# Optimization experiments

Measured on AMD Instinct MI355X. Metric: run time of the kernel, lower is better.

## Reference

```python
import jax, jax.numpy as jnp
import numpy as np

EPS = 1e-5

def _conv(x, w, b):
    # NCHW x OIHW -> NCHW, stride 1, SAME padding (stencil center (1,1) of 3x3, or 1x1)
    y = jax.lax.conv_general_dilated(x, w, (1, 1), 'SAME',
                                     dimension_numbers=('NCHW', 'OIHW', 'NCHW'))
    return y + b[None, :, None, None]

def _bn(x, gamma, beta):
    # training-mode batchnorm: stats over (N, H, W) per channel
    mean = jnp.mean(x, axis=(0, 2, 3), keepdims=True)
    var = jnp.var(x, axis=(0, 2, 3), keepdims=True)
    xhat = (x - mean) * jax.lax.rsqrt(var + EPS)
    return xhat * gamma[None, :, None, None] + beta[None, :, None, None]

def setup_inputs() -> dict:
    key = jax.random.key(0)
    ks = jax.random.split(key, 12)
    B, Cin, Cout, H, W = 2, 64, 64, 512, 512
    s = 0.05
    return {
        'x':  jax.random.normal(ks[0], (B, Cin, H, W), jnp.float32),
        'w1': jax.random.normal(ks[1], (Cout, Cin, 3, 3), jnp.float32) * s,
        'b1': jnp.zeros((Cout,), jnp.float32),
        'g1': jnp.ones((Cout,), jnp.float32),
        'be1': jnp.zeros((Cout,), jnp.float32),
        'w2': jax.random.normal(ks[2], (Cout, Cout, 3, 3), jnp.float32) * s,
        'b2': jnp.zeros((Cout,), jnp.float32),
        'g2': jnp.ones((Cout,), jnp.float32),
        'be2': jnp.zeros((Cout,), jnp.float32),
        'wp': jax.random.normal(ks[3], (Cout, Cin, 1, 1), jnp.float32) * s,
        'bp': jnp.zeros((Cout,), jnp.float32),
        'gp': jnp.ones((Cout,), jnp.float32),
        'bep': jnp.zeros((Cout,), jnp.float32),
    }

def reference(x, w1, b1, g1, be1, w2, b2, g2, be2, wp, bp, gp, bep):
    # project branch: 1x1 conv ([(0,0)] stencil) + BN
    residual = _bn(_conv(x, wp, bp), gp, bep)
    # conv1: pad + 3x3 lattice conv (full cp stencil) + BN + Identity downsample + ReLU
    out = jax.nn.relu(_bn(_conv(x, w1, b1), g1, be1))
    # conv2: pad + 3x3 lattice conv + BN
    out = _bn(_conv(out, w2, b2), g2, be2)
    # residual add + output ReLU
    return jax.nn.relu(out + residual)
```

## Files before the change

### kernel.cpp

```cpp
#include <hip/hip_runtime.h>
#include <hip/hip_bf16.h>
#include <stdint.h>

typedef short short8 __attribute__((ext_vector_type(8)));
typedef float f32x4 __attribute__((ext_vector_type(4)));
typedef unsigned int u32;
typedef unsigned short u16;

#define HH 512
#define WW 512
#define CC 64
#define PLANE (HH*WW)
#define NSTATF 524288.0f

#define KTW 32
#define HSTR1 560
#define KBSTR1 1120
#define SLOTB1 4480
#define NSLOT 6
#define RING1 (NSLOT*SLOTB1)
#define BOUNCE1 16384
#define BOUNCE2 8192
#define NBC1 1024
#define K5S 132

__device__ __forceinline__ u16 f2bf(float f) {
  __hip_bfloat16 h = __float2bfloat16(f);
  return __builtin_bit_cast(u16, h);
}
__device__ __forceinline__ u32 pk2bf(float a, float b) {
  return (u32)f2bf(a) | ((u32)f2bf(b) << 16);
}
__device__ __forceinline__ float bf2f(u16 u) {
  u32 x = ((u32)u) << 16;
  return __builtin_bit_cast(float, x);
}
__device__ __forceinline__ int m6(int v) {
  v -= (v >= 6) ? 6 : 0;
  v -= (v >= 6) ? 6 : 0;
  return v;
}
__device__ __forceinline__ void lds_barrier() {
  asm volatile("s_waitcnt lgkmcnt(0)" ::: "memory");
  __builtin_amdgcn_s_barrier();
  __builtin_amdgcn_sched_barrier(0);
}

__global__ __launch_bounds__(512) void kprep(const float* __restrict__ w1,
    const float* __restrict__ w2, const float* __restrict__ wp,
    u16* __restrict__ wb1, u16* __restrict__ wb2, u16* __restrict__ wbp)
{
  const int id = blockIdx.x*512 + threadIdx.x;
  const int lane = id & 63;
  if (id < 9216) {
    const float* w = (id < 4608) ? w1 : w2;
    u16* o = (id < 4608) ? wb1 : wb2;
    const int fid = (id < 4608) ? (id >> 6) : ((id - 4608) >> 6);
    const int ct4 = fid / 18, rem = fid % 18;
    const int tap = rem >> 1, kb = rem & 1;
    const int cout = ct4*16 + (lane & 15);
    const int k0c = kb*32 + (lane >> 4)*8;
    u32 ow[4];
#pragma unroll
    for (int p = 0; p < 4; ++p) {
      ow[p] = pk2bf(w[(size_t)(cout*64 + k0c + p*2)*9 + tap],
                    w[(size_t)(cout*64 + k0c + p*2 + 1)*9 + tap]);
    }
    *(uint4*)(o + ((size_t)fid*64 + lane)*8) = make_uint4(ow[0],ow[1],ow[2],ow[3]);
  } else if (id < 9728) {
    const int fid = (id - 9216) >> 6;
    const int ct4 = fid >> 1, kb = fid & 1;
    const int cout = ct4*16 + (lane & 15);
    const int k0c = kb*32 + (lane >> 4)*8;
    u32 ow[4];
#pragma unroll
    for (int p = 0; p < 4; ++p)
      ow[p] = pk2bf(wp[cout*64 + k0c + p*2], wp[cout*64 + k0c + p*2 + 1]);
    *(uint4*)(wbp + ((size_t)fid*64 + lane)*8) = make_uint4(ow[0],ow[1],ow[2],ow[3]);
  }
}

__global__ __launch_bounds__(256) void k0(const float* __restrict__ x, u16* __restrict__ xh)
{
  __shared__ __align__(16) u32 Tp[32*260];
  const int tid = threadIdx.x;
  const int wt = blockIdx.x, h = blockIdx.y, n = blockIdx.z;
  const int w0 = wt*256;
  const float* xp = x + (size_t)n*CC*PLANE + (size_t)h*WW + w0;
#pragma unroll
  for (int it = 0; it < 8; ++it) {
    const int j = it*256 + tid;
    const int c2 = j >> 6, w4 = (j & 63) << 2;
    const f32x4 a = *(const f32x4*)(xp + (size_t)(c2*2    )*PLANE + w4);
    const f32x4 b = *(const f32x4*)(xp + (size_t)(c2*2 + 1)*PLANE + w4);
    uint4 o;
    o.x = pk2bf(a[0], b[0]);
    o.y = pk2bf(a[1], b[1]);
    o.z = pk2bf(a[2], b[2]);
    o.w = pk2bf(a[3], b[3]);
    *(uint4*)(Tp + (u32)c2*260 + (u32)(w4 ^ (4*(c2 >> 2)))) = o;
  }
  __syncthreads();
  u16* op = xh + ((size_t)(n*HH + h)*WW + w0)*CC;
#pragma unroll
  for (int it = 0; it < 8; ++it) {
    const int j = it*256 + tid;
    const int w = j >> 3, c8 = j & 7;
    const u32 wsw = (u32)(w ^ (4*c8));
    uint4 o;
    o.x = Tp[(u32)(c8*4 + 0)*260 + wsw];
    o.y = Tp[(u32)(c8*4 + 1)*260 + wsw];
    o.z = Tp[(u32)(c8*4 + 2)*260 + wsw];
    o.w = Tp[(u32)(c8*4 + 3)*260 + wsw];
    *(uint4*)(op + (size_t)w*CC + c8*8) = o;
  }
}

__global__ __launch_bounds__(256, 2) void kconv1(const u16* __restrict__ in,
    const u16* __restrict__ wb, const u16* __restrict__ wbp,
    u16* __restrict__ out, u16* __restrict__ yp,
    float* __restrict__ ps, float* __restrict__ pq,
    float* __restrict__ psp, float* __restrict__ pqp)
{
  __shared__ __align__(16) char LB[RING1 + BOUNCE1 + 512];
  const int tid = threadIdx.x;
  const int lane = tid & 63, wv = tid >> 6;
  const int l15 = lane & 15, lq = lane >> 4;
  const int wt = blockIdx.x, hs = blockIdx.y, n = blockIdx.z;
  const int w0 = wt*KTW, h0 = hs*16;
  const int bid = (n*32 + hs)*16 + wt;

  short8 wfr[18];
#pragma unroll
  for (int f = 0; f < 18; ++f)
    wfr[f] = *(const short8*)(wb + ((size_t)(wv*18 + f)*64 + lane)*8);
  short8 wpf[2];
#pragma unroll
  for (int kb = 0; kb < 2; ++kb)
    wpf[kb] = *(const short8*)(wbp + ((size_t)(wv*2 + kb)*64 + lane)*8);

  float s4[4] = {0,0,0,0}, q4[4] = {0,0,0,0};
  float sp4[4] = {0,0,0,0}, qp4[4] = {0,0,0,0};
  const u16* inb = in + (size_t)n*PLANE*CC;
  const u32 co0 = (u32)((lq >> 1)*KBSTR1 + (lq & 1)*HSTR1);
  const u32 co1 = co0 + 2*KBSTR1;

  auto ld_one = [&](int j, int cl, int c8) -> uint4 {
    const int gh = h0 - 1 + j, gw = w0 - 1 + cl;
    if (((u32)gh < (u32)HH) && ((u32)gw < (u32)WW))
      return *(const uint4*)(inb + ((size_t)gh*WW + gw)*CC + c8*8);
    return make_uint4(0u,0u,0u,0u);
  };
  auto st_one = [&](int slot, int cl, int c8, uint4 v) {
    *(uint4*)(LB + (size_t)slot*SLOTB1 + (c8>>1)*KBSTR1 + (c8&1)*HSTR1 + cl*16) = v;
  };

  for (int idx = tid; idx < 4*272; idx += 256) {
    const int jj = idx / 272, rem = idx - jj*272;
    st_one(jj, rem >> 3, rem & 7, ld_one(jj, rem >> 3, rem & 7));
  }
  __syncthreads();

  uint4 st0, st1, st2;
  auto issue2 = [&](int jb) {
    { const int idx = tid;       const int jj = idx/272, rem = idx - jj*272;
      st0 = ld_one(jb + jj, rem >> 3, rem & 7); }
    { const int idx = 256 + tid; const int jj = idx/272, rem = idx - jj*272;
      st1 = ld_one(jb + jj, rem >> 3, rem & 7); }
    if (tid < 32) { const int idx = 512 + tid; const int jj = idx/272, rem = idx - jj*272;
      st2 = ld_one(jb + jj, rem >> 3, rem & 7); }
  };
  auto write2 = [&](int jb) {
    { const int idx = tid;       const int jj = idx/272, rem = idx - jj*272;
      st_one(m6(jb + jj), rem >> 3, rem & 7, st0); }
    { const int idx = 256 + tid; const int jj = idx/272, rem = idx - jj*272;
      st_one(m6(jb + jj), rem >> 3, rem & 7, st1); }
    if (tid < 32) { const int idx = 512 + tid; const int jj = idx/272, rem = idx - jj*272;
      st_one(m6(jb + jj), rem >> 3, rem & 7, st2); }
  };

  issue2(4);

  for (int g = 0; g < 8; ++g) {
    if (g > 0) write2(2*g + 2);
    lds_barrier();
    if (g < 7) issue2(2*g + 4);

    const char* sb[4];
#pragma unroll
    for (int mi = 0; mi < 4; ++mi)
      sb[mi] = LB + (size_t)m6(2*g + mi)*SLOTB1 + l15*16;
    f32x4 a0t0, a0t1, a1t0, a1t1;
    f32x4 p0t0, p0t1, p1t0, p1t1;
#pragma unroll
    for (int r = 0; r < 4; ++r) {
      a0t0[r]=0.f; a0t1[r]=0.f; a1t0[r]=0.f; a1t1[r]=0.f;
      p0t0[r]=0.f; p0t1[r]=0.f; p1t0[r]=0.f; p1t1[r]=0.f;
    }
#pragma unroll
    for (int t = 0; t < 2; ++t) {
      const int pb = t*16;
#pragma unroll
      for (int kb = 0; kb < 2; ++kb) {
        const u32 ck = kb ? co1 : co0;
#pragma unroll
        for (int mi = 0; mi < 4; ++mi) {
#pragma unroll
          for (int kw = 0; kw < 3; ++kw) {
            const short8 X = *(const short8*)(sb[mi] + ck + (u32)((pb + kw)*16));
            if (mi <= 2) {
              const short8 Wf = wfr[(mi*3 + kw)*2 + kb];
              if (t == 0) a0t0 = __builtin_amdgcn_mfma_f32_16x16x32_bf16(Wf, X, a0t0, 0,0,0);
              else        a0t1 = __builtin_amdgcn_mfma_f32_16x16x32_bf16(Wf, X, a0t1, 0,0,0);
            }
            if (mi >= 1) {
              const short8 Wf = wfr[((mi-1)*3 + kw)*2 + kb];
              if (t == 0) a1t0 = __builtin_amdgcn_mfma_f32_16x16x32_bf16(Wf, X, a1t0, 0,0,0);
              else        a1t1 = __builtin_amdgcn_mfma_f32_16x16x32_bf16(Wf, X, a1t1, 0,0,0);
            }
            if (kw == 1 && mi == 1) {
              if (t == 0) p0t0 = __builtin_amdgcn_mfma_f32_16x16x32_bf16(wpf[kb], X, p0t0, 0,0,0);
              else        p0t1 = __builtin_amdgcn_mfma_f32_16x16x32_bf16(wpf[kb], X, p0t1, 0,0,0);
            }
            if (kw == 1 && mi == 2) {
              if (t == 0) p1t0 = __builtin_amdgcn_mfma_f32_16x16x32_bf16(wpf[kb], X, p1t0, 0,0,0);
              else        p1t1 = __builtin_amdgcn_mfma_f32_16x16x32_bf16(wpf[kb], X, p1t1, 0,0,0);
            }
          }
        }
      }
    }
    {
      const int co = wv*16 + lq*4;
#pragma unroll
      for (int r = 0; r < 4; ++r) {
        s4[r] += a0t0[r] + a0t1[r] + a1t0[r] + a1t1[r];
        q4[r] = fmaf(a0t0[r], a0t0[r], q4[r]);
        q4[r] = fmaf(a0t1[r], a0t1[r], q4[r]);
        q4[r] = fmaf(a1t0[r], a1t0[r], q4[r]);
        q4[r] = fmaf(a1t1[r], a1t1[r], q4[r]);
        sp4[r] += p0t0[r] + p0t1[r] + p1t0[r] + p1t1[r];
        qp4[r] = fmaf(p0t0[r], p0t0[r], qp4[r]);
        qp4[r] = fmaf(p0t1[r], p0t1[r], qp4[r]);
        qp4[r] = fmaf(p1t0[r], p1t0[r], qp4[r]);
        qp4[r] = fmaf(p1t1[r], p1t1[r], qp4[r]);
      }
#pragma unroll
      for (int t = 0; t < 2; ++t) {
        const int pos = t*16 + l15;
        const u32 addr = ((u32)(pos*128 + co*2)) ^ (((u32)(pos & 7)) << 4);
        uint2 c0, c1, d0, d1;
        if (t == 0) {
          c0.x = pk2bf(a0t0[0], a0t0[1]); c0.y = pk2bf(a0t0[2], a0t0[3]);
          c1.x = pk2bf(a1t0[0], a1t0[1]); c1.y = pk2bf(a1t0[2], a1t0[3]);
          d0.x = pk2bf(p0t0[0], p0t0[1]); d0.y = pk2bf(p0t0[2], p0t0[3]);
          d1.x = pk2bf(p1t0[0], p1t0[1]); d1.y = pk2bf(p1t0[2], p1t0[3]);
        } else {
          c0.x = pk2bf(a0t1[0], a0t1[1]); c0.y = pk2bf(a0t1[2], a0t1[3]);
          c1.x = pk2bf(a1t1[0], a1t1[1]); c1.y = pk2bf(a1t1[2], a1t1[3]);
          d0.x = pk2bf(p0t1[0], p0t1[1]); d0.y = pk2bf(p0t1[2], p0t1[3]);
          d1.x = pk2bf(p1t1[0], p1t1[1]); d1.y = pk2bf(p1t1[2], p1t1[3]);
        }
        *(uint2*)(LB + RING1 + 0*4096 + addr) = c0;
        *(uint2*)(LB + RING1 + 1*4096 + addr) = c1;
        *(uint2*)(LB + RING1 + 2*4096 + addr) = d0;
        *(uint2*)(LB + RING1 + 3*4096 + addr) = d1;
      }
    }
    lds_barrier();
    {
      const int rowi = tid >> 6, tt = tid & 63;
      const int pos = tt >> 1, half = (tt & 1)*64;
      const char* bb = LB + RING1 + rowi*4096;
      u16* base = (rowi < 2) ? out : yp;
      const int orow = h0 + 2*g + (rowi & 1);
      char* dst = (char*)base + ((size_t)((n*HH + orow)*WW + w0 + pos))*128 + half;
      const u32 sw = ((u32)(pos & 7)) << 4;
#pragma unroll
      for (int k2 = 0; k2 < 4; ++k2) {
        const uint4 v = *(const uint4*)(bb + (((u32)(pos*128 + half + k2*16)) ^ sw));
        *(uint4*)(dst + k2*16) = v;
      }
    }
  }

#pragma unroll
  for (int d = 1; d <= 8; d <<= 1) {
#pragma unroll
    for (int r = 0; r < 4; ++r) {
      s4[r] += __shfl_xor(s4[r], d, 64);
      q4[r] += __shfl_xor(q4[r], d, 64);
      sp4[r] += __shfl_xor(sp4[r], d, 64);
      qp4[r] += __shfl_xor(qp4[r], d, 64);
    }
  }
  if (l15 == 0) {
#pragma unroll
    for (int r = 0; r < 4; ++r) {
      const int co = wv*16 + lq*4 + r;
      ps[(size_t)co*NBC1 + bid] = s4[r];
      pq[(size_t)co*NBC1 + bid] = q4[r];
      psp[(size_t)co*NBC1 + bid] = sp4[r];
      pqp[(size_t)co*NBC1 + bid] = qp4[r];
    }
  }
}

__global__ __launch_bounds__(256, 2) void kconv2(const u16* __restrict__ in,
    const u16* __restrict__ wb,
    const float* __restrict__ As, const float* __restrict__ Bs,
    u16* __restrict__ out, float* __restrict__ ps, float* __restrict__ pq)
{
  __shared__ __align__(16) char LB[RING1 + BOUNCE2 + 512];
  float* sA = (float*)(LB + RING1 + BOUNCE2);
  float* sB = sA + 64;
  const int tid = threadIdx.x;
  const int lane = tid & 63, wv = tid >> 6;
  const int l15 = lane & 15, lq = lane >> 4;
  const int wt = blockIdx.x, hs = blockIdx.y, n = blockIdx.z;
  const int w0 = wt*KTW, h0 = hs*16;
  const int bid = (n*32 + hs)*16 + wt;

  if (tid < 64) { sA[tid] = As[tid]; sB[tid] = Bs[tid]; }
  __syncthreads();

  short8 wfr[18];
#pragma unroll
  for (int f = 0; f < 18; ++f)
    wfr[f] = *(const short8*)(wb + ((size_t)(wv*18 + f)*64 + lane)*8);

  float s4[4] = {0,0,0,0}, q4[4] = {0,0,0,0};
  const u16* inb = in + (size_t)n*PLANE*CC;
  const u32 co0 = (u32)((lq >> 1)*KBSTR1 + (lq & 1)*HSTR1);
  const u32 co1 = co0 + 2*KBSTR1;

  auto ld_one = [&](int j, int cl, int c8) -> uint4 {
    const int gh = h0 - 1 + j, gw = w0 - 1 + cl;
    if (((u32)gh < (u32)HH) && ((u32)gw < (u32)WW))
      return *(const uint4*)(inb + ((size_t)gh*WW + gw)*CC + c8*8);
    return make_uint4(0u,0u,0u,0u);
  };
  auto st_one = [&](int slot, int cl, int c8, uint4 v) {
    const u32* uw = (const u32*)&v;
    u32 ow[4];
    const int cb = c8*8;
#pragma unroll
    for (int h2 = 0; h2 < 4; ++h2) {
      float f0 = fmaxf(bf2f((u16)(uw[h2] & 0xFFFFu)) * sA[cb+h2*2]   + sB[cb+h2*2],   0.f);
      float f1 = fmaxf(bf2f((u16)(uw[h2] >> 16))     * sA[cb+h2*2+1] + sB[cb+h2*2+1], 0.f);
      ow[h2] = pk2bf(f0, f1);
    }
    *(uint4*)(LB + (size_t)slot*SLOTB1 + (c8>>1)*KBSTR1 + (c8&1)*HSTR1 + cl*16) =
        make_uint4(ow[0],ow[1],ow[2],ow[3]);
  };

  for (int idx = tid; idx < 4*272; idx += 256) {
    const int jj = idx / 272, rem = idx - jj*272;
    st_one(jj, rem >> 3, rem & 7, ld_one(jj, rem >> 3, rem & 7));
  }
  __syncthreads();

  uint4 st0, st1, st2;
  auto issue2 = [&](int jb) {
    { const int idx = tid;       const int jj = idx/272, rem = idx - jj*272;
      st0 = ld_one(jb + jj, rem >> 3, rem & 7); }
    { const int idx = 256 + tid; const int jj = idx/272, rem = idx - jj*272;
      st1 = ld_one(jb + jj, rem >> 3, rem & 7); }
    if (tid < 32) { const int idx = 512 + tid; const int jj = idx/272, rem = idx - jj*272;
      st2 = ld_one(jb + jj, rem >> 3, rem & 7); }
  };
  auto write2 = [&](int jb) {
    { const int idx = tid;       const int jj = idx/272, rem = idx - jj*272;
      st_one(m6(jb + jj), rem >> 3, rem & 7, st0); }
    { const int idx = 256 + tid; const int jj = idx/272, rem = idx - jj*272;
      st_one(m6(jb + jj), rem >> 3, rem & 7, st1); }
    if (tid < 32) { const int idx = 512 + tid; const int jj = idx/272, rem = idx - jj*272;
      st_one(m6(jb + jj), rem >> 3, rem & 7, st2); }
  };

  issue2(4);

  for (int g = 0; g < 8; ++g) {
    if (g > 0) write2(2*g + 2);
    lds_barrier();
    if (g < 7) issue2(2*g + 4);

    const char* sb[4];
#pragma unroll
    for (int mi = 0; mi < 4; ++mi)
      sb[mi] = LB + (size_t)m6(2*g + mi)*SLOTB1 + l15*16;
    f32x4 a0t0, a0t1, a1t0, a1t1;
#pragma unroll
    for (int r = 0; r < 4; ++r) { a0t0[r]=0.f; a0t1[r]=0.f; a1t0[r]=0.f; a1t1[r]=0.f; }
#pragma unroll
    for (int t = 0; t < 2; ++t) {
      const int pb = t*16;
#pragma unroll
      for (int kb = 0; kb < 2; ++kb) {
        const u32 ck = kb ? co1 : co0;
#pragma unroll
        for (int mi = 0; mi < 4; ++mi) {
#pragma unroll
          for (int kw = 0; kw < 3; ++kw) {
            const short8 X = *(const short8*)(sb[mi] + ck + (u32)((pb + kw)*16));
            if (mi <= 2) {
              const short8 Wf = wfr[(mi*3 + kw)*2 + kb];
              if (t == 0) a0t0 = __builtin_amdgcn_mfma_f32_16x16x32_bf16(Wf, X, a0t0, 0,0,0);
              else        a0t1 = __builtin_amdgcn_mfma_f32_16x16x32_bf16(Wf, X, a0t1, 0,0,0);
            }
            if (mi >= 1) {
              const short8 Wf = wfr[((mi-1)*3 + kw)*2 + kb];
              if (t == 0) a1t0 = __builtin_amdgcn_mfma_f32_16x16x32_bf16(Wf, X, a1t0, 0,0,0);
              else        a1t1 = __builtin_amdgcn_mfma_f32_16x16x32_bf16(Wf, X, a1t1, 0,0,0);
            }
          }
        }
      }
    }
    {
      const int co = wv*16 + lq*4;
#pragma unroll
      for (int r = 0; r < 4; ++r) {
        s4[r] += a0t0[r] + a0t1[r] + a1t0[r] + a1t1[r];
        q4[r] = fmaf(a0t0[r], a0t0[r], q4[r]);
        q4[r] = fmaf(a0t1[r], a0t1[r], q4[r]);
        q4[r] = fmaf(a1t0[r], a1t0[r], q4[r]);
        q4[r] = fmaf(a1t1[r], a1t1[r], q4[r]);
      }
#pragma unroll
      for (int t = 0; t < 2; ++t) {
        const int pos = t*16 + l15;
        const u32 addr = ((u32)(pos*128 + co*2)) ^ (((u32)(pos & 7)) << 4);
        uint2 c0, c1;
        if (t == 0) {
          c0.x = pk2bf(a0t0[0], a0t0[1]); c0.y = pk2bf(a0t0[2], a0t0[3]);
          c1.x = pk2bf(a1t0[0], a1t0[1]); c1.y = pk2bf(a1t0[2], a1t0[3]);
        } else {
          c0.x = pk2bf(a0t1[0], a0t1[1]); c0.y = pk2bf(a0t1[2], a0t1[3]);
          c1.x = pk2bf(a1t1[0], a1t1[1]); c1.y = pk2bf(a1t1[2], a1t1[3]);
        }
        *(uint2*)(LB + RING1 + 0*4096 + addr) = c0;
        *(uint2*)(LB + RING1 + 1*4096 + addr) = c1;
      }
    }
    lds_barrier();
    {
      const int rowi = tid >> 7, tt = tid & 127;
      const int pos = tt >> 2, qb = (tt & 3)*32;
      const char* bb = LB + RING1 + rowi*4096;
      const u32 a0 = ((u32)(pos*128 + qb)) ^ (((u32)(pos & 7)) << 4);
      const uint4 v0 = *(const uint4*)(bb + a0);
      const uint4 v1 = *(const uint4*)(bb + (a0 ^ 16u));
      char* dst = (char*)out + ((size_t)((n*HH + h0 + 2*g + rowi)*WW + w0 + pos))*128 + qb;
      *(uint4*)dst = v0;
      *(uint4*)(dst + 16) = v1;
    }
  }

#pragma unroll
  for (int d = 1; d <= 8; d <<= 1) {
#pragma unroll
    for (int r = 0; r < 4; ++r) {
      s4[r] += __shfl_xor(s4[r], d, 64);
      q4[r] += __shfl_xor(q4[r], d, 64);
    }
  }
  if (l15 == 0) {
#pragma unroll
    for (int r = 0; r < 4; ++r) {
      const int co = wv*16 + lq*4 + r;
      ps[(size_t)co*NBC1 + bid] = s4[r];
      pq[(size_t)co*NBC1 + bid] = q4[r];
    }
  }
}

__global__ __launch_bounds__(256) void kfin2(
    const float* __restrict__ psA, const float* __restrict__ pqA,
    const float* __restrict__ gA, const float* __restrict__ beA,
    float* __restrict__ AA, float* __restrict__ BA, int cntA,
    const float* __restrict__ psB, const float* __restrict__ pqB,
    const float* __restrict__ gB, const float* __restrict__ beB,
    float* __restrict__ AB, float* __restrict__ BB, int cntB)
{
  const int blk = blockIdx.x;
  const bool second = blk >= 64;
  const int c = blk & 63;
  const float* psx = second ? psB : psA;
  const float* pqx = second ? pqB : pqA;
  const float* g  = second ? gB  : gA;
  const float* be = second ? beB : beA;
  float* A  = second ? AB : AA;
  float* Bc = second ? BB : BA;
  const int cnt = second ? cntB : cntA;

  const int t = threadIdx.x;
  float sv = 0.f, s2 = 0.f;
  const float* pr = psx + (size_t)c*cnt;
  const float* qr = pqx + (size_t)c*cnt;
  for (int k = t; k < cnt; k += 256) { sv += pr[k]; s2 += qr[k]; }
#pragma unroll
  for (int d = 1; d < 64; d <<= 1) { sv += __shfl_xor(sv, d, 64); s2 += __shfl_xor(s2, d, 64); }
  __shared__ float as_[4], aq_[4];
  if ((t & 63) == 0) { as_[t >> 6] = sv; aq_[t >> 6] = s2; }
  __syncthreads();
  if (t == 0) {
    sv = as_[0] + as_[1] + as_[2] + as_[3];
    s2 = aq_[0] + aq_[1] + aq_[2] + aq_[3];
    const float mean = sv / NSTATF;
    const float var = s2 / NSTATF - mean*mean;
    const float istd = rsqrtf(var + 1e-5f);
    const float a = g[c] * istd;
    A[c] = a;
    Bc[c] = be[c] - mean * a;
  }
}

__global__ __launch_bounds__(256) void k5(const u16* __restrict__ y2, const u16* __restrict__ yp,
    const float* __restrict__ A2, const float* __restrict__ B2c,
    const float* __restrict__ Ap, const float* __restrict__ Bp,
    float* __restrict__ outp)
{
  __shared__ float T[CC*K5S];
  __shared__ float cA2[64], cB2[64], cAp[64], cBp[64];
  const int tid = threadIdx.x;
  const int lane = tid & 63, wv = tid >> 6;
  const int wt = blockIdx.x, h = blockIdx.y, n = blockIdx.z;
  const int w0 = wt*128;
  if (tid < 64) { cA2[tid] = A2[tid]; cB2[tid] = B2c[tid]; cAp[tid] = Ap[tid]; cBp[tid] = Bp[tid]; }
  __syncthreads();
  const u16* p2 = y2 + ((size_t)(n*HH + h)*WW + w0)*CC;
  const u16* pp = yp + ((size_t)(n*HH + h)*WW + w0)*CC;
#pragma unroll
  for (int it = 0; it < 4; ++it) {
    const int j = it*256 + tid;
    const int w = j >> 3, c8 = j & 7;
    const uint4 u2 = *(const uint4*)(p2 + (size_t)w*CC + c8*8);
    const uint4 up = *(const uint4*)(pp + (size_t)w*CC + c8*8);
    const u32* m2 = (const u32*)&u2;
    const u32* mp = (const u32*)&up;
    const u32 sw = ((u32)(c8 & 3)) << 3;
#pragma unroll
    for (int h2 = 0; h2 < 4; ++h2) {
      const int c = c8*8 + h2*2;
      const float a = bf2f((u16)(m2[h2] & 0xFFFFu)), b = bf2f((u16)(m2[h2] >> 16));
      const float ra = bf2f((u16)(mp[h2] & 0xFFFFu)), rb = bf2f((u16)(mp[h2] >> 16));
      const u32 wsw = (u32)w ^ sw;
      T[(u32)(c    )*K5S + wsw] = fmaxf(a*cA2[c]   + cB2[c]   + ra*cAp[c]   + cBp[c],   0.f);
      T[(u32)(c + 1)*K5S + wsw] = fmaxf(b*cA2[c+1] + cB2[c+1] + rb*cAp[c+1] + cBp[c+1], 0.f);
    }
  }
  __syncthreads();
#pragma unroll
  for (int cc = 0; cc < 16; ++cc) {
    const int c = cc*4 + wv;
    const u32 sw = ((u32)((c >> 3) & 3)) << 3;
    const u32 idx = (u32)c*K5S + (((u32)(lane*2)) ^ sw);
    float2 v;
    v.x = T[idx];
    v.y = T[idx + 1];
    *(float2*)(outp + ((size_t)((n*CC + c)*HH + h))*WW + w0 + lane*2) = v;
  }
}

extern "C" void kernel_launch(void* const* d_in, const int* in_sizes, int n_in,
                              void* d_out, int out_size, void* d_ws, size_t ws_size,
                              hipStream_t stream)
{
  (void)in_sizes; (void)n_in; (void)out_size;
  const float* x   = (const float*)d_in[0];
  const float* w1  = (const float*)d_in[1];
  const float* g1  = (const float*)d_in[3];
  const float* be1 = (const float*)d_in[4];
  const float* w2  = (const float*)d_in[5];
  const float* g2  = (const float*)d_in[7];
  const float* be2 = (const float*)d_in[8];
  const float* wp  = (const float*)d_in[9];
  const float* gp  = (const float*)d_in[11];
  const float* bep = (const float*)d_in[12];

  const size_t TENB = (size_t)2*CC*PLANE*2;
  char* ws = (char*)d_ws;
  u16* bufA = (u16*)ws;
  u16* bufB = (u16*)(ws + TENB);
  u16* bufC = (u16*)(ws + TENB*2);
  char* aux = ws + TENB*3;
  u16* wb1 = (u16*)aux;
  u16* wb2 = (u16*)(aux + 73728);
  u16* wbp = (u16*)(aux + 147456);
  float* ps1 = (float*)(aux + 155648);
  float* pq1 = ps1 + 64*NBC1;
  float* psp = pq1 + 64*NBC1;
  float* pqp = psp + 64*NBC1;
  float* ps2 = pqp + 64*NBC1;
  float* pq2 = ps2 + 64*NBC1;
  float* A1  = pq2 + 64*NBC1;
  float* B1  = A1 + 64;
  float* A2  = B1 + 64;
  float* B2c = A2 + 64;
  float* Ap  = B2c + 64;
  float* Bp  = Ap + 64;
  const size_t need = (size_t)(Bp + 64 - (float*)ws) * 4;
  if (ws_size < need) return;

  kprep<<<19, 512, 0, stream>>>(w1, w2, wp, wb1, wb2, wbp);
  k0<<<dim3(2, HH, 2), 256, 0, stream>>>(x, bufA);
  kconv1<<<dim3(16, 32, 2), 256, 0, stream>>>(bufA, wb1, wbp,
                                              bufB, bufC, ps1, pq1, psp, pqp);
  kfin2<<<128, 256, 0, stream>>>(ps1, pq1, g1, be1, A1, B1, NBC1,
                                 psp, pqp, gp, bep, Ap, Bp, NBC1);
  kconv2<<<dim3(16, 32, 2), 256, 0, stream>>>(bufB, wb2, A1, B1,
                                              bufA, ps2, pq2);
  kfin2<<<64, 256, 0, stream>>>(ps2, pq2, g2, be2, A2, B2c, NBC1,
                                ps2, pq2, g2, be2, A2, B2c, NBC1);
  k5<<<dim3(4, HH, 2), 256, 0, stream>>>(bufA, bufC, A2, B2c, Ap, Bp, (float*)d_out);
}
```

Measured before the change: 216.3 us.

## Recompute 1x1 projection in final kernel instead of storing it

The projection conv output is no longer written to a global buffer in kconv1. Instead, k5 reloads the bf16 NHWC input and recomputes the 1x1 conv with MFMA before the fused BN/residual/ReLU epilogue. kconv2 now writes to bufC so bufA (the transposed input) stays live. This trades a full-size bf16 write and read of the projection tensor for a re-read of the input plus a small amount of extra matrix work and more LDS use in k5.

```diff
diff --git a/kernel.cpp b/kernel.cpp
--- a/kernel.cpp
+++ b/kernel.cpp
@@ -19,8 +19,7 @@
 #define SLOTB1 4480
 #define NSLOT 6
 #define RING1 (NSLOT*SLOTB1)
-#define BOUNCE1 16384
-#define BOUNCE2 8192
+#define BOUNCE 8192
 #define NBC1 1024
 #define K5S 132
 
@@ -118,11 +117,11 @@
 
 __global__ __launch_bounds__(256, 2) void kconv1(const u16* __restrict__ in,
     const u16* __restrict__ wb, const u16* __restrict__ wbp,
-    u16* __restrict__ out, u16* __restrict__ yp,
+    u16* __restrict__ out,
     float* __restrict__ ps, float* __restrict__ pq,
     float* __restrict__ psp, float* __restrict__ pqp)
 {
-  __shared__ __align__(16) char LB[RING1 + BOUNCE1 + 512];
+  __shared__ __align__(16) char LB[RING1 + BOUNCE + 512];
   const int tid = threadIdx.x;
   const int lane = tid & 63, wv = tid >> 6;
   const int l15 = lane & 15, lq = lane >> 4;
@@ -249,38 +248,29 @@
       for (int t = 0; t < 2; ++t) {
         const int pos = t*16 + l15;
         const u32 addr = ((u32)(pos*128 + co*2)) ^ (((u32)(pos & 7)) << 4);
-        uint2 c0, c1, d0, d1;
+        uint2 c0, c1;
         if (t == 0) {
           c0.x = pk2bf(a0t0[0], a0t0[1]); c0.y = pk2bf(a0t0[2], a0t0[3]);
           c1.x = pk2bf(a1t0[0], a1t0[1]); c1.y = pk2bf(a1t0[2], a1t0[3]);
-          d0.x = pk2bf(p0t0[0], p0t0[1]); d0.y = pk2bf(p0t0[2], p0t0[3]);
-          d1.x = pk2bf(p1t0[0], p1t0[1]); d1.y = pk2bf(p1t0[2], p1t0[3]);
         } else {
           c0.x = pk2bf(a0t1[0], a0t1[1]); c0.y = pk2bf(a0t1[2], a0t1[3]);
           c1.x = pk2bf(a1t1[0], a1t1[1]); c1.y = pk2bf(a1t1[2], a1t1[3]);
-          d0.x = pk2bf(p0t1[0], p0t1[1]); d0.y = pk2bf(p0t1[2], p0t1[3]);
-          d1.x = pk2bf(p1t1[0], p1t1[1]); d1.y = pk2bf(p1t1[2], p1t1[3]);
         }
         *(uint2*)(LB + RING1 + 0*4096 + addr) = c0;
         *(uint2*)(LB + RING1 + 1*4096 + addr) = c1;
-        *(uint2*)(LB + RING1 + 2*4096 + addr) = d0;
-        *(uint2*)(LB + RING1 + 3*4096 + addr) = d1;
       }
     }
     lds_barrier();
     {
-      const int rowi = tid >> 6, tt = tid & 63;
-      const int pos = tt >> 1, half = (tt & 1)*64;
+      const int rowi = tid >> 7, tt = tid & 127;
+      const int pos = tt >> 2, qb = (tt & 3)*32;
       const char* bb = LB + RING1 + rowi*4096;
-      u16* base = (rowi < 2) ? out : yp;
-      const int orow = h0 + 2*g + (rowi & 1);
-      char* dst = (char*)base + ((size_t)((n*HH + orow)*WW + w0 + pos))*128 + half;
-      const u32 sw = ((u32)(pos & 7)) << 4;
-#pragma unroll
-      for (int k2 = 0; k2 < 4; ++k2) {
-        const uint4 v = *(const uint4*)(bb + (((u32)(pos*128 + half + k2*16)) ^ sw));
-        *(uint4*)(dst + k2*16) = v;
-      }
+      const u32 a0 = ((u32)(pos*128 + qb)) ^ (((u32)(pos & 7)) << 4);
+      const uint4 v0 = *(const uint4*)(bb + a0);
+      const uint4 v1 = *(const uint4*)(bb + (a0 ^ 16u));
+      char* dst = (char*)out + ((size_t)((n*HH + h0 + 2*g + rowi)*WW + w0 + pos))*128 + qb;
+      *(uint4*)dst = v0;
+      *(uint4*)(dst + 16) = v1;
     }
   }
 
@@ -311,8 +301,8 @@
     const float* __restrict__ As, const float* __restrict__ Bs,
     u16* __restrict__ out, float* __restrict__ ps, float* __restrict__ pq)
 {
-  __shared__ __align__(16) char LB[RING1 + BOUNCE2 + 512];
-  float* sA = (float*)(LB + RING1 + BOUNCE2);
+  __shared__ __align__(16) char LB[RING1 + BOUNCE + 512];
+  float* sA = (float*)(LB + RING1 + BOUNCE);
   float* sB = sA + 64;
   const int tid = threadIdx.x;
   const int lane = tid & 63, wv = tid >> 6;
@@ -516,27 +506,67 @@
   }
 }
 
-__global__ __launch_bounds__(256) void k5(const u16* __restrict__ y2, const u16* __restrict__ yp,
+__global__ __launch_bounds__(256) void k5(const u16* __restrict__ y2, const u16* __restrict__ xh,
+    const u16* __restrict__ wbp,
     const float* __restrict__ A2, const float* __restrict__ B2c,
     const float* __restrict__ Ap, const float* __restrict__ Bp,
     float* __restrict__ outp)
 {
-  __shared__ float T[CC*K5S];
-  __shared__ float cA2[64], cB2[64], cAp[64], cBp[64];
+  __shared__ __align__(16) char L5[50176 + 1024];
+  float* T = (float*)L5;
+  char* SG = L5;
+  char* BN = L5 + 33792;
+  float* cA2 = (float*)(L5 + 50176);
+  float* cB2 = cA2 + 64;
+  float* cAp = cB2 + 64;
+  float* cBp = cAp + 64;
   const int tid = threadIdx.x;
   const int lane = tid & 63, wv = tid >> 6;
+  const int l15 = lane & 15, lq = lane >> 4;
   const int wt = blockIdx.x, h = blockIdx.y, n = blockIdx.z;
   const int w0 = wt*128;
   if (tid < 64) { cA2[tid] = A2[tid]; cB2[tid] = B2c[tid]; cAp[tid] = Ap[tid]; cBp[tid] = Bp[tid]; }
+
+  short8 wpf[2];
+#pragma unroll
+  for (int kb = 0; kb < 2; ++kb)
+    wpf[kb] = *(const short8*)(wbp + ((size_t)(wv*2 + kb)*64 + lane)*8);
+
+  const u16* px = xh + ((size_t)(n*HH + h)*WW + w0)*CC;
+#pragma unroll
+  for (int it = 0; it < 4; ++it) {
+    const int j = it*256 + tid;
+    const int w = j >> 3, c8 = j & 7;
+    const uint4 v = *(const uint4*)(px + (size_t)w*CC + c8*8);
+    *(uint4*)(SG + (((u32)(w*128 + c8*16)) ^ (((u32)(w & 7)) << 4))) = v;
+  }
+  __syncthreads();
+  {
+    const int co = wv*16 + lq*4;
+#pragma unroll
+    for (int t = 0; t < 8; ++t) {
+      const int pos = t*16 + l15;
+      const u32 sw = ((u32)(pos & 7)) << 4;
+      f32x4 acc = {0.f, 0.f, 0.f, 0.f};
+#pragma unroll
+      for (int kb = 0; kb < 2; ++kb) {
+        const short8 X = *(const short8*)(SG + (((u32)(pos*128 + kb*64 + lq*16)) ^ sw));
+        acc = __builtin_amdgcn_mfma_f32_16x16x32_bf16(wpf[kb], X, acc, 0, 0, 0);
+      }
+      uint2 d;
+      d.x = pk2bf(acc[0], acc[1]);
+      d.y = pk2bf(acc[2], acc[3]);
+      *(uint2*)(BN + (((u32)(pos*128 + co*2)) ^ sw)) = d;
+    }
+  }
   __syncthreads();
   const u16* p2 = y2 + ((size_t)(n*HH + h)*WW + w0)*CC;
-  const u16* pp = yp + ((size_t)(n*HH + h)*WW + w0)*CC;
 #pragma unroll
   for (int it = 0; it < 4; ++it) {
     const int j = it*256 + tid;
     const int w = j >> 3, c8 = j & 7;
     const uint4 u2 = *(const uint4*)(p2 + (size_t)w*CC + c8*8);
-    const uint4 up = *(const uint4*)(pp + (size_t)w*CC + c8*8);
+    const uint4 up = *(const uint4*)(BN + (((u32)(w*128 + c8*16)) ^ (((u32)(w & 7)) << 4)));
     const u32* m2 = (const u32*)&u2;
     const u32* mp = (const u32*)&up;
     const u32 sw = ((u32)(c8 & 3)) << 3;
@@ -606,12 +636,12 @@
   kprep<<<19, 512, 0, stream>>>(w1, w2, wp, wb1, wb2, wbp);
   k0<<<dim3(2, HH, 2), 256, 0, stream>>>(x, bufA);
   kconv1<<<dim3(16, 32, 2), 256, 0, stream>>>(bufA, wb1, wbp,
-                                              bufB, bufC, ps1, pq1, psp, pqp);
+                                              bufB, ps1, pq1, psp, pqp);
   kfin2<<<128, 256, 0, stream>>>(ps1, pq1, g1, be1, A1, B1, NBC1,
                                  psp, pqp, gp, bep, Ap, Bp, NBC1);
   kconv2<<<dim3(16, 32, 2), 256, 0, stream>>>(bufB, wb2, A1, B1,
-                                              bufA, ps2, pq2);
+                                              bufC, ps2, pq2);
   kfin2<<<64, 256, 0, stream>>>(ps2, pq2, g2, be2, A2, B2c, NBC1,
                                 ps2, pq2, g2, be2, A2, B2c, NBC1);
-  k5<<<dim3(4, HH, 2), 256, 0, stream>>>(bufA, bufC, A2, B2c, Ap, Bp, (float*)d_out);
-}
+  k5<<<dim3(4, HH, 2), 256, 0, stream>>>(bufC, bufA, wbp, A2, B2c, Ap, Bp, (float*)d_out);
+}
```

Result: faster. 209.9 us, median of 2 (-3.0%).
